# Kernel tuning notes

Measured on AMD Instinct MI355X. Metric: run time of the kernel, lower is better.

## Reference

```python
import jax, jax.numpy as jnp
import numpy as np

E = 16      # num_experts
H = 1024    # hidden_size
O = 1       # output_size
B = 4096    # batch
K = 2       # top-k (hard-coded in module)


def setup_inputs() -> dict:
    key = jax.random.key(0)
    ks = jax.random.split(key, 7)
    s_h = 1.0 / np.sqrt(H)
    inp = {
        "embeddings": jax.random.normal(ks[0], (B, H), dtype=jnp.float32),
        "router_w": jax.random.uniform(ks[1], (H, E), jnp.float32, -s_h, s_h),
        "router_b": jax.random.uniform(ks[2], (E,), jnp.float32, -s_h, s_h),
        "w1": jax.random.uniform(ks[3], (E, H, H), jnp.float32, -s_h, s_h),
        "b1": jax.random.uniform(ks[4], (E, H), jnp.float32, -s_h, s_h),
        "w2": jax.random.uniform(ks[5], (E, H, O), jnp.float32, -s_h, s_h),
        "b2": jax.random.uniform(ks[6], (E, O), jnp.float32, -s_h, s_h),
    }
    return inp


def reference(embeddings, router_w, router_b, w1, b1, w2, b2):
    # Router: top-2 experts per token, softmax over the 2 selected logits.
    logits = embeddings @ router_w + router_b                 # [B, E]
    top_vals, top_idx = jax.lax.top_k(logits, K)              # [B, K]
    top_w = jax.nn.softmax(top_vals, axis=-1)                 # [B, K]

    # Per-expert combine weight: w_e[b] = sum_k top_w[b,k] * (top_idx[b,k]==e)
    onehot = (top_idx[:, :, None] == jnp.arange(E)[None, None, :])  # [B, K, E]
    comb = jnp.einsum('bk,bke->eb', top_w, onehot.astype(top_w.dtype))  # [E, B]

    # Dense per-expert 2-layer MLP (small fixed E); masked-weighted combine
    # reproduces the gather/scatter-add exactly.
    h = jax.nn.relu(jnp.einsum('bh,ehd->ebd', embeddings, w1) + b1[:, None, :])  # [E, B, H]
    out = jnp.einsum('ebd,edo->ebo', h, w2) + b2[:, None, :]                      # [E, B, O]
    prediction = jnp.einsum('eb,ebo->bo', comb, out)                              # [B, O]
    return prediction
```

## Files before the change

### kernel.cpp

```cpp
#include <hip/hip_runtime.h>
#include <hip/hip_bf16.h>
#include <stdint.h>

#define E_EXP 16
#define H_DIM 1024
#define B_TOK 4096
#define NS 4
#define BM 128
#define BN 256
#define BK 64
#define KS 16
#define KC 64
#define RTM 128
#define RSTRIDE (KC + 4)

typedef short bf16x8 __attribute__((ext_vector_type(8)));
typedef float f32x4 __attribute__((ext_vector_type(4)));

__device__ __forceinline__ unsigned short f2bf(float x) {
  union { float f; unsigned u; } v; v.f = x;
  unsigned r = v.u + 0x7FFFu + ((v.u >> 16) & 1u);
  return (unsigned short)(r >> 16);
}

__device__ __forceinline__ void gload_lds16(const void* g, void* l) {
  __builtin_amdgcn_global_load_lds(
      (const __attribute__((address_space(1))) void*)g,
      (__attribute__((address_space(3))) void*)l, 16, 0, 0);
}

__global__ __launch_bounds__(256) void k_router_gemm(
    const float* __restrict__ emb, const float* __restrict__ rw,
    unsigned short* __restrict__ emb_bf, float* __restrict__ part)
{
  __shared__ float embL[RTM * RSTRIDE];
  __shared__ float rwL[KC * E_EXP];

  const int t0 = blockIdx.x * RTM;
  const int ks = blockIdx.y;
  const int tid = threadIdx.x;

#pragma unroll
  for (int it = 0; it < 8; ++it) {
    const int i = tid + 256 * it;
    const int row = i >> 4;
    const int c4 = i & 15;
    const size_t goff = (size_t)(t0 + row) * H_DIM + ks * KC + c4 * 4;
    const f32x4 v = *(const f32x4*)(emb + goff);
    ushort4 o;
    o.x = f2bf(v[0]); o.y = f2bf(v[1]); o.z = f2bf(v[2]); o.w = f2bf(v[3]);
    *(ushort4*)(emb_bf + goff) = o;
    *(f32x4*)(embL + row * RSTRIDE + c4 * 4) = v;
  }
  {
    const f32x4 v = *(const f32x4*)(rw + (size_t)ks * (KC * E_EXP) + tid * 4);
    *(f32x4*)(rwL + tid * 4) = v;
  }
  __syncthreads();

  const int w = tid >> 6, lane = tid & 63;
  const int tg = lane & 15, eg = lane >> 4;
  const int ta = w * 32 + tg, tb = ta + 16;

  f32x4 accA = {0.f, 0.f, 0.f, 0.f};
  f32x4 accB = {0.f, 0.f, 0.f, 0.f};
#pragma unroll
  for (int k4 = 0; k4 < KC / 4; ++k4) {
    const f32x4 e0 = *(const f32x4*)(embL + ta * RSTRIDE + k4 * 4);
    const f32x4 e1 = *(const f32x4*)(embL + tb * RSTRIDE + k4 * 4);
#pragma unroll
    for (int h = 0; h < 4; ++h) {
      const f32x4 r = *(const f32x4*)(rwL + (k4 * 4 + h) * E_EXP + eg * 4);
      accA += e0[h] * r;
      accB += e1[h] * r;
    }
  }

  *(f32x4*)(part + ((size_t)ks * B_TOK + t0 + ta) * E_EXP + eg * 4) = accA;
  *(f32x4*)(part + ((size_t)ks * B_TOK + t0 + tb) * E_EXP + eg * 4) = accB;
}

__global__ __launch_bounds__(256) void k_router_select(
    const float* __restrict__ part, const float* __restrict__ rb,
    int* __restrict__ counts, int* __restrict__ lists,
    int4* __restrict__ meta, float2* __restrict__ wts)
{
  __shared__ int lcnt[E_EXP];
  __shared__ int base[E_EXP];
  const int tid = threadIdx.x;
  const int t = blockIdx.x * 256 + tid;
  if (tid < E_EXP) lcnt[tid] = 0;

  float lg[16];
#pragma unroll
  for (int q = 0; q < 4; ++q) {
    const f32x4 b = *(const f32x4*)(rb + q * 4);
    lg[q * 4 + 0] = b[0]; lg[q * 4 + 1] = b[1];
    lg[q * 4 + 2] = b[2]; lg[q * 4 + 3] = b[3];
  }
#pragma unroll
  for (int s = 0; s < KS; ++s) {
#pragma unroll
    for (int q = 0; q < 4; ++q) {
      const f32x4 v = *(const f32x4*)(part + ((size_t)s * B_TOK + t) * E_EXP + q * 4);
      lg[q * 4 + 0] += v[0]; lg[q * 4 + 1] += v[1];
      lg[q * 4 + 2] += v[2]; lg[q * 4 + 3] += v[3];
    }
  }

  float best = -1e30f; int b0 = 0;
#pragma unroll
  for (int e = 0; e < 16; ++e)
    if (lg[e] > best) { best = lg[e]; b0 = e; }
  float best2 = -1e30f; int b1i = 0;
#pragma unroll
  for (int e = 0; e < 16; ++e)
    if (e != b0 && lg[e] > best2) { best2 = lg[e]; b1i = e; }

  __syncthreads();
  const int l0 = atomicAdd(&lcnt[b0], 1);
  const int l1 = atomicAdd(&lcnt[b1i], 1);
  __syncthreads();
  if (tid < E_EXP) base[tid] = atomicAdd(&counts[tid], lcnt[tid]);
  __syncthreads();

  const int p0 = base[b0] + l0;
  const int p1 = base[b1i] + l1;
  lists[b0 * B_TOK + p0] = t;
  lists[b1i * B_TOK + p1] = t;
  meta[t] = make_int4(b0, b1i, p0, p1);
  const float e1v = expf(best2 - best);
  const float w0 = 1.f / (1.f + e1v);
  wts[t] = make_float2(w0, e1v * w0);
}

__global__ __launch_bounds__(256) void k_w1t(const float* __restrict__ w1,
                                             unsigned short* __restrict__ w1t)
{
  __shared__ unsigned short tile[64][65];
  const int e = blockIdx.z;
  const int ht = blockIdx.x, dt = blockIdx.y;
  const float* src = w1 + ((size_t)e * H_DIM + ht * 64) * H_DIM + dt * 64;
  const int tr = threadIdx.x >> 4;
  const int tc = threadIdx.x & 15;
#pragma unroll
  for (int i = 0; i < 4; ++i) {
    const int r = tr + i * 16;
    const float4 v = *(const float4*)(src + (size_t)r * H_DIM + tc * 4);
    tile[r][tc * 4 + 0] = f2bf(v.x);
    tile[r][tc * 4 + 1] = f2bf(v.y);
    tile[r][tc * 4 + 2] = f2bf(v.z);
    tile[r][tc * 4 + 3] = f2bf(v.w);
  }
  __syncthreads();
  unsigned short* dst = w1t + ((size_t)e * H_DIM + dt * 64) * H_DIM + ht * 64;
  const int wr = threadIdx.x >> 3;
  const int wc = threadIdx.x & 7;
#pragma unroll
  for (int i = 0; i < 2; ++i) {
    const int r = wr + i * 32;
    ushort4 t0, t1;
    t0.x = tile[wc * 8 + 0][r]; t0.y = tile[wc * 8 + 1][r];
    t0.z = tile[wc * 8 + 2][r]; t0.w = tile[wc * 8 + 3][r];
    t1.x = tile[wc * 8 + 4][r]; t1.y = tile[wc * 8 + 5][r];
    t1.z = tile[wc * 8 + 6][r]; t1.w = tile[wc * 8 + 7][r];
    *(ushort4*)(dst + (size_t)r * H_DIM + wc * 8) = t0;
    *(ushort4*)(dst + (size_t)r * H_DIM + wc * 8 + 4) = t1;
  }
}

__global__ __launch_bounds__(512, 4) void k_moe_gemm(
    const unsigned short* __restrict__ emb_bf,
    const unsigned short* __restrict__ w1t,
    const float* __restrict__ b1, const float* __restrict__ w2,
    const int* __restrict__ counts, const int* __restrict__ lists,
    float* __restrict__ outbuf)
{
  const int bid = blockIdx.x;
  const int xcd = bid & 7;
  const int j = bid >> 3;
  const int e = xcd + 8 * (j >> 7);
  const int r = j & 127;
  const int ns = r >> 5;
  const int mb = r & 31;
  const int cnt = counts[e];
  if (mb * BM >= cnt) return;

  __shared__ unsigned short lA[BM * BK];
  __shared__ unsigned short lB[BN * BK];
  __shared__ int toks[BM];

  const int tid = threadIdx.x;
  const int w = tid >> 6, lane = tid & 63;

  if (tid < BM) {
    const int p = mb * BM + tid;
    toks[tid] = lists[e * B_TOK + (p < cnt ? p : 0)];
  }
  __syncthreads();

  const unsigned short* w1te = w1t + ((size_t)e * H_DIM + ns * BN) * H_DIM;

  f32x4 acc[4][4];
#pragma unroll
  for (int m = 0; m < 4; ++m)
#pragma unroll
    for (int n = 0; n < 4; ++n) acc[m][n] = (f32x4){0.f, 0.f, 0.f, 0.f};

  const int scb = ((lane & 7) * 16) ^ ((lane >> 3) << 4);
  const int wm = w >> 2, wn = w & 3;
  const int lr = lane & 15, lg = lane >> 4;

  for (int k0 = 0; k0 < H_DIM; k0 += BK) {
#pragma unroll
    for (int i = 0; i < 2; ++i) {
      const int chunk = w * 2 + i;
      const int row = chunk * 8 + (lane >> 3);
      const unsigned short* src = emb_bf + (size_t)toks[row] * H_DIM + k0 + (scb >> 1);
      gload_lds16(src, (char*)lA + chunk * 1024);
    }
#pragma unroll
    for (int i = 0; i < 4; ++i) {
      const int chunk = w * 4 + i;
      const int n = chunk * 8 + (lane >> 3);
      const unsigned short* src = w1te + (size_t)n * H_DIM + k0 + (scb >> 1);
      gload_lds16(src, (char*)lB + chunk * 1024);
    }
    __syncthreads();

#pragma unroll
    for (int kk = 0; kk < 2; ++kk) {
      const int kb = kk * 64 + lg * 16;
      bf16x8 af[4], bfr[4];
#pragma unroll
      for (int m = 0; m < 4; ++m) {
        const int row = wm * 64 + m * 16 + lr;
        af[m] = *(const bf16x8*)((const char*)lA + row * 128 + (kb ^ ((row & 7) << 4)));
      }
#pragma unroll
      for (int n = 0; n < 4; ++n) {
        const int row = wn * 64 + n * 16 + lr;
        bfr[n] = *(const bf16x8*)((const char*)lB + row * 128 + (kb ^ ((row & 7) << 4)));
      }
#pragma unroll
      for (int m = 0; m < 4; ++m)
#pragma unroll
        for (int n = 0; n < 4; ++n)
          acc[m][n] = __builtin_amdgcn_mfma_f32_16x16x32_bf16(af[m], bfr[n], acc[m][n], 0, 0, 0);
    }
    __syncthreads();
  }

  const float* b1e = b1 + (size_t)e * H_DIM + ns * BN;
  const float* w2e = w2 + (size_t)e * H_DIM + ns * BN;

  float rs[4][4];
#pragma unroll
  for (int m = 0; m < 4; ++m)
#pragma unroll
    for (int r4 = 0; r4 < 4; ++r4) rs[m][r4] = 0.f;

#pragma unroll
  for (int n = 0; n < 4; ++n) {
    const int d = wn * 64 + n * 16 + lr;
    const float bb = b1e[d];
    const float ww = w2e[d];
#pragma unroll
    for (int m = 0; m < 4; ++m)
#pragma unroll
      for (int r4 = 0; r4 < 4; ++r4) {
        float v = acc[m][n][r4] + bb;
        v = fmaxf(v, 0.f);
        rs[m][r4] = fmaf(v, ww, rs[m][r4]);
      }
  }
#pragma unroll
  for (int mask = 8; mask >= 1; mask >>= 1) {
#pragma unroll
    for (int m = 0; m < 4; ++m)
#pragma unroll
      for (int r4 = 0; r4 < 4; ++r4) rs[m][r4] += __shfl_xor(rs[m][r4], mask, 64);
  }

  if (lr == 0) {
    float* ob = outbuf + (((size_t)ns * 4 + wn) * E_EXP + e) * B_TOK + mb * BM;
#pragma unroll
    for (int m = 0; m < 4; ++m)
#pragma unroll
      for (int r4 = 0; r4 < 4; ++r4)
        ob[wm * 64 + m * 16 + lg * 4 + r4] = rs[m][r4];
  }
}

__global__ __launch_bounds__(256) void k_combine(
    const int4* __restrict__ meta, const float2* __restrict__ wts,
    const float* __restrict__ outbuf, const float* __restrict__ b2,
    float* __restrict__ out)
{
  const int t = blockIdx.x * 256 + threadIdx.x;
  if (t >= B_TOK) return;
  const int4 m = meta[t];
  const float2 w = wts[t];
  float o0 = b2[m.x], o1 = b2[m.y];
#pragma unroll
  for (int s = 0; s < NS * 4; ++s) {
    o0 += outbuf[((size_t)s * E_EXP + m.x) * B_TOK + m.z];
    o1 += outbuf[((size_t)s * E_EXP + m.y) * B_TOK + m.w];
  }
  out[t] = w.x * o0 + w.y * o1;
}

extern "C" void kernel_launch(void* const* d_in, const int* in_sizes, int n_in,
                              void* d_out, int out_size, void* d_ws, size_t ws_size,
                              hipStream_t stream)
{
  const float* emb = (const float*)d_in[0];
  const float* rw  = (const float*)d_in[1];
  const float* rb  = (const float*)d_in[2];
  const float* w1  = (const float*)d_in[3];
  const float* b1  = (const float*)d_in[4];
  const float* w2  = (const float*)d_in[5];
  const float* b2  = (const float*)d_in[6];
  float* out = (float*)d_out;

  char* ws = (char*)d_ws;
  size_t cur = 0;
  auto alloc = [&](size_t bytes) -> void* {
    void* p = ws + cur;
    cur += (bytes + 255) & ~(size_t)255;
    return p;
  };
  int*            counts = (int*)alloc(64);
  int4*           meta   = (int4*)alloc((size_t)B_TOK * 16);
  float2*         wts    = (float2*)alloc((size_t)B_TOK * 8);
  int*            lists  = (int*)alloc((size_t)E_EXP * B_TOK * 4);
  float*          outbuf = (float*)alloc((size_t)NS * 4 * E_EXP * B_TOK * 4);
  float*          part   = (float*)alloc((size_t)KS * B_TOK * E_EXP * 4);
  unsigned short* emb_bf = (unsigned short*)alloc((size_t)B_TOK * H_DIM * 2);
  unsigned short* w1t    = (unsigned short*)alloc((size_t)E_EXP * H_DIM * H_DIM * 2);

  hipMemsetAsync(counts, 0, 64, stream);
  k_router_gemm<<<dim3(B_TOK / RTM, KS), 256, 0, stream>>>(emb, rw, emb_bf, part);
  k_router_select<<<B_TOK / 256, 256, 0, stream>>>(part, rb, counts, lists, meta, wts);
  k_w1t<<<dim3(16, 16, 16), 256, 0, stream>>>(w1, w1t);
  k_moe_gemm<<<dim3((B_TOK / BM) * NS * E_EXP), 512, 0, stream>>>(emb_bf, w1t, b1, w2, counts, lists, outbuf);
  k_combine<<<B_TOK / 256, 256, 0, stream>>>(meta, wts, outbuf, b2, out);
}
```

Before: 91.42 us.

## Double-buffer LDS tiles in MoE GEMM to overlap global loads with MFMA

```diff
diff --git a/kernel.cpp b/kernel.cpp
--- a/kernel.cpp
+++ b/kernel.cpp
@@ -169,7 +169,7 @@
   }
 }
 
-__global__ __launch_bounds__(512, 4) void k_moe_gemm(
+__global__ __launch_bounds__(512, 2) void k_moe_gemm(
     const unsigned short* __restrict__ emb_bf,
     const unsigned short* __restrict__ w1t,
     const float* __restrict__ b1, const float* __restrict__ w2,
@@ -186,8 +186,7 @@
   const int cnt = counts[e];
   if (mb * BM >= cnt) return;
 
-  __shared__ unsigned short lA[BM * BK];
-  __shared__ unsigned short lB[BN * BK];
+  __shared__ unsigned short ldsbuf[2][(BM + BN) * BK];
   __shared__ int toks[BM];
 
   const int tid = threadIdx.x;
@@ -201,33 +200,42 @@
 
   const unsigned short* w1te = w1t + ((size_t)e * H_DIM + ns * BN) * H_DIM;
 
+  const int scb = ((lane & 7) * 16) ^ ((lane >> 3) << 4);
+
+  const unsigned short* aSrc[2];
+#pragma unroll
+  for (int i = 0; i < 2; ++i) {
+    const int row = (w * 2 + i) * 8 + (lane >> 3);
+    aSrc[i] = emb_bf + (size_t)toks[row] * H_DIM + (scb >> 1);
+  }
+  const unsigned short* bSrc[4];
+#pragma unroll
+  for (int i = 0; i < 4; ++i) {
+    const int n = (w * 4 + i) * 8 + (lane >> 3);
+    bSrc[i] = w1te + (size_t)n * H_DIM + (scb >> 1);
+  }
+
   f32x4 acc[4][4];
 #pragma unroll
   for (int m = 0; m < 4; ++m)
 #pragma unroll
     for (int n = 0; n < 4; ++n) acc[m][n] = (f32x4){0.f, 0.f, 0.f, 0.f};
 
-  const int scb = ((lane & 7) * 16) ^ ((lane >> 3) << 4);
   const int wm = w >> 2, wn = w & 3;
   const int lr = lane & 15, lg = lane >> 4;
 
-  for (int k0 = 0; k0 < H_DIM; k0 += BK) {
-#pragma unroll
-    for (int i = 0; i < 2; ++i) {
-      const int chunk = w * 2 + i;
-      const int row = chunk * 8 + (lane >> 3);
-      const unsigned short* src = emb_bf + (size_t)toks[row] * H_DIM + k0 + (scb >> 1);
-      gload_lds16(src, (char*)lA + chunk * 1024);
-    }
-#pragma unroll
-    for (int i = 0; i < 4; ++i) {
-      const int chunk = w * 4 + i;
-      const int n = chunk * 8 + (lane >> 3);
-      const unsigned short* src = w1te + (size_t)n * H_DIM + k0 + (scb >> 1);
-      gload_lds16(src, (char*)lB + chunk * 1024);
-    }
-    __syncthreads();
-
+  auto stage = [&](int buf, int k0) {
+    char* base = (char*)ldsbuf[buf];
+#pragma unroll
+    for (int i = 0; i < 2; ++i)
+      gload_lds16(aSrc[i] + k0, base + (w * 2 + i) * 1024);
+#pragma unroll
+    for (int i = 0; i < 4; ++i)
+      gload_lds16(bSrc[i] + k0, base + 16384 + (w * 4 + i) * 1024);
+  };
+
+  auto compute = [&](int buf) {
+    const char* base = (const char*)ldsbuf[buf];
 #pragma unroll
     for (int kk = 0; kk < 2; ++kk) {
       const int kb = kk * 64 + lg * 16;
@@ -235,21 +243,35 @@
 #pragma unroll
       for (int m = 0; m < 4; ++m) {
         const int row = wm * 64 + m * 16 + lr;
-        af[m] = *(const bf16x8*)((const char*)lA + row * 128 + (kb ^ ((row & 7) << 4)));
+        af[m] = *(const bf16x8*)(base + row * 128 + (kb ^ ((row & 7) << 4)));
       }
 #pragma unroll
       for (int n = 0; n < 4; ++n) {
         const int row = wn * 64 + n * 16 + lr;
-        bfr[n] = *(const bf16x8*)((const char*)lB + row * 128 + (kb ^ ((row & 7) << 4)));
+        bfr[n] = *(const bf16x8*)(base + 16384 + row * 128 + (kb ^ ((row & 7) << 4)));
       }
+      __builtin_amdgcn_s_setprio(1);
 #pragma unroll
       for (int m = 0; m < 4; ++m)
 #pragma unroll
         for (int n = 0; n < 4; ++n)
           acc[m][n] = __builtin_amdgcn_mfma_f32_16x16x32_bf16(af[m], bfr[n], acc[m][n], 0, 0, 0);
+      __builtin_amdgcn_s_setprio(0);
     }
+  };
+
+  stage(0, 0);
+  __syncthreads();
+
+  int cur = 0;
+#pragma unroll 1
+  for (int t = 0; t < H_DIM / BK - 1; ++t) {
+    stage(cur ^ 1, (t + 1) * BK);
+    compute(cur);
     __syncthreads();
-  }
+    cur ^= 1;
+  }
+  compute(cur);
 
   const float* b1e = b1 + (size_t)e * H_DIM + ns * BN;
   const float* w2e = w2 + (size_t)e * H_DIM + ns * BN;
```

Result: no change. 90.43 us (-1.1%).

## Restructure MoE GEMM into persistent 128x64 tiles looping over token blocks

Applied to the files above, without the earlier changes.

```diff
diff --git a/kernel.cpp b/kernel.cpp
--- a/kernel.cpp
+++ b/kernel.cpp
@@ -5,10 +5,10 @@
 #define E_EXP 16
 #define H_DIM 1024
 #define B_TOK 4096
-#define NS 4
-#define BM 128
-#define BN 256
 #define BK 64
+#define GBM 128
+#define GBN 64
+#define NSLOT 32
 #define KS 16
 #define KC 64
 #define RTM 128
@@ -169,7 +169,7 @@
   }
 }
 
-__global__ __launch_bounds__(512, 4) void k_moe_gemm(
+__global__ __launch_bounds__(256, 4) void k_moe_gemm(
     const unsigned short* __restrict__ emb_bf,
     const unsigned short* __restrict__ w1t,
     const float* __restrict__ b1, const float* __restrict__ w2,
@@ -179,116 +179,125 @@
   const int bid = blockIdx.x;
   const int xcd = bid & 7;
   const int j = bid >> 3;
-  const int e = xcd + 8 * (j >> 7);
-  const int r = j & 127;
-  const int ns = r >> 5;
-  const int mb = r & 31;
+  const int e  = xcd + 8 * (j >> 7);
+  const int r  = j & 127;
+  const int nb = r >> 3;
+  const int mbg = r & 7;
   const int cnt = counts[e];
-  if (mb * BM >= cnt) return;
-
-  __shared__ unsigned short lA[BM * BK];
-  __shared__ unsigned short lB[BN * BK];
-  __shared__ int toks[BM];
+
+  __shared__ unsigned short lA[GBM * BK];
+  __shared__ unsigned short lB[GBN * BK];
+  __shared__ int toks[GBM];
 
   const int tid = threadIdx.x;
   const int w = tid >> 6, lane = tid & 63;
-
-  if (tid < BM) {
-    const int p = mb * BM + tid;
-    toks[tid] = lists[e * B_TOK + (p < cnt ? p : 0)];
-  }
-  __syncthreads();
-
-  const unsigned short* w1te = w1t + ((size_t)e * H_DIM + ns * BN) * H_DIM;
-
-  f32x4 acc[4][4];
-#pragma unroll
-  for (int m = 0; m < 4; ++m)
-#pragma unroll
-    for (int n = 0; n < 4; ++n) acc[m][n] = (f32x4){0.f, 0.f, 0.f, 0.f};
-
   const int scb = ((lane & 7) * 16) ^ ((lane >> 3) << 4);
-  const int wm = w >> 2, wn = w & 3;
+  const int wm = w >> 1, wn = w & 1;
   const int lr = lane & 15, lg = lane >> 4;
 
-  for (int k0 = 0; k0 < H_DIM; k0 += BK) {
-#pragma unroll
-    for (int i = 0; i < 2; ++i) {
-      const int chunk = w * 2 + i;
-      const int row = chunk * 8 + (lane >> 3);
-      const unsigned short* src = emb_bf + (size_t)toks[row] * H_DIM + k0 + (scb >> 1);
-      gload_lds16(src, (char*)lA + chunk * 1024);
-    }
+  const unsigned short* w1tb = w1t + ((size_t)e * H_DIM + nb * GBN) * H_DIM;
+  const float* b1e = b1 + (size_t)e * H_DIM + nb * GBN;
+  const float* w2e = w2 + (size_t)e * H_DIM + nb * GBN;
+
+  const unsigned short* bSrc[2];
+#pragma unroll
+  for (int i = 0; i < 2; ++i) {
+    const int n = (w * 2 + i) * 8 + (lane >> 3);
+    bSrc[i] = w1tb + (size_t)n * H_DIM + (scb >> 1);
+  }
+
+  for (int mb = mbg; mb * GBM < cnt; mb += 8) {
+    if (tid < GBM) {
+      const int p = mb * GBM + tid;
+      toks[tid] = lists[e * B_TOK + (p < cnt ? p : 0)];
+    }
+    __syncthreads();
+
+    const unsigned short* aSrc[4];
 #pragma unroll
     for (int i = 0; i < 4; ++i) {
-      const int chunk = w * 4 + i;
-      const int n = chunk * 8 + (lane >> 3);
-      const unsigned short* src = w1te + (size_t)n * H_DIM + k0 + (scb >> 1);
-      gload_lds16(src, (char*)lB + chunk * 1024);
+      const int row = (w * 4 + i) * 8 + (lane >> 3);
+      aSrc[i] = emb_bf + (size_t)toks[row] * H_DIM + (scb >> 1);
+    }
+
+    f32x4 acc[4][2];
+#pragma unroll
+    for (int m = 0; m < 4; ++m)
+#pragma unroll
+      for (int n = 0; n < 2; ++n) acc[m][n] = (f32x4){0.f, 0.f, 0.f, 0.f};
+
+    for (int k0 = 0; k0 < H_DIM; k0 += BK) {
+#pragma unroll
+      for (int i = 0; i < 4; ++i)
+        gload_lds16(aSrc[i] + k0, (char*)lA + (w * 4 + i) * 1024);
+#pragma unroll
+      for (int i = 0; i < 2; ++i)
+        gload_lds16(bSrc[i] + k0, (char*)lB + (w * 2 + i) * 1024);
+      __syncthreads();
+
+#pragma unroll
+      for (int kk = 0; kk < 2; ++kk) {
+        const int kb = kk * 64 + lg * 16;
+        bf16x8 af[4], bfr[2];
+#pragma unroll
+        for (int m = 0; m < 4; ++m) {
+          const int row = wm * 64 + m * 16 + lr;
+          af[m] = *(const bf16x8*)((const char*)lA + row * 128 + (kb ^ ((row & 7) << 4)));
+        }
+#pragma unroll
+        for (int n = 0; n < 2; ++n) {
+          const int row = wn * 32 + n * 16 + lr;
+          bfr[n] = *(const bf16x8*)((const char*)lB + row * 128 + (kb ^ ((row & 7) << 4)));
+        }
+        __builtin_amdgcn_s_setprio(1);
+#pragma unroll
+        for (int m = 0; m < 4; ++m)
+#pragma unroll
+          for (int n = 0; n < 2; ++n)
+            acc[m][n] = __builtin_amdgcn_mfma_f32_16x16x32_bf16(af[m], bfr[n], acc[m][n], 0, 0, 0);
+        __builtin_amdgcn_s_setprio(0);
+      }
+      __syncthreads();
+    }
+
+    float rs[4][4];
+#pragma unroll
+    for (int m = 0; m < 4; ++m)
+#pragma unroll
+      for (int r4 = 0; r4 < 4; ++r4) rs[m][r4] = 0.f;
+
+#pragma unroll
+    for (int n = 0; n < 2; ++n) {
+      const int d = wn * 32 + n * 16 + lr;
+      const float bb = b1e[d];
+      const float ww = w2e[d];
+#pragma unroll
+      for (int m = 0; m < 4; ++m)
+#pragma unroll
+        for (int r4 = 0; r4 < 4; ++r4) {
+          float v = acc[m][n][r4] + bb;
+          v = fmaxf(v, 0.f);
+          rs[m][r4] = fmaf(v, ww, rs[m][r4]);
+        }
+    }
+#pragma unroll
+    for (int mask = 8; mask >= 1; mask >>= 1) {
+#pragma unroll
+      for (int m = 0; m < 4; ++m)
+#pragma unroll
+        for (int r4 = 0; r4 < 4; ++r4) rs[m][r4] += __shfl_xor(rs[m][r4], mask, 64);
+    }
+
+    if (lr == 0) {
+      const int slot = nb * 2 + wn;
+      float* ob = outbuf + ((size_t)slot * E_EXP + e) * B_TOK + mb * GBM;
+#pragma unroll
+      for (int m = 0; m < 4; ++m)
+#pragma unroll
+        for (int r4 = 0; r4 < 4; ++r4)
+          ob[wm * 64 + m * 16 + lg * 4 + r4] = rs[m][r4];
     }
     __syncthreads();
-
-#pragma unroll
-    for (int kk = 0; kk < 2; ++kk) {
-      const int kb = kk * 64 + lg * 16;
-      bf16x8 af[4], bfr[4];
-#pragma unroll
-      for (int m = 0; m < 4; ++m) {
-        const int row = wm * 64 + m * 16 + lr;
-        af[m] = *(const bf16x8*)((const char*)lA + row * 128 + (kb ^ ((row & 7) << 4)));
-      }
-#pragma unroll
-      for (int n = 0; n < 4; ++n) {
-        const int row = wn * 64 + n * 16 + lr;
-        bfr[n] = *(const bf16x8*)((const char*)lB + row * 128 + (kb ^ ((row & 7) << 4)));
-      }
-#pragma unroll
-      for (int m = 0; m < 4; ++m)
-#pragma unroll
-        for (int n = 0; n < 4; ++n)
-          acc[m][n] = __builtin_amdgcn_mfma_f32_16x16x32_bf16(af[m], bfr[n], acc[m][n], 0, 0, 0);
-    }
-    __syncthreads();
-  }
-
-  const float* b1e = b1 + (size_t)e * H_DIM + ns * BN;
-  const float* w2e = w2 + (size_t)e * H_DIM + ns * BN;
-
-  float rs[4][4];
-#pragma unroll
-  for (int m = 0; m < 4; ++m)
-#pragma unroll
-    for (int r4 = 0; r4 < 4; ++r4) rs[m][r4] = 0.f;
-
-#pragma unroll
-  for (int n = 0; n < 4; ++n) {
-    const int d = wn * 64 + n * 16 + lr;
-    const float bb = b1e[d];
-    const float ww = w2e[d];
-#pragma unroll
-    for (int m = 0; m < 4; ++m)
-#pragma unroll
-      for (int r4 = 0; r4 < 4; ++r4) {
-        float v = acc[m][n][r4] + bb;
-        v = fmaxf(v, 0.f);
-        rs[m][r4] = fmaf(v, ww, rs[m][r4]);
-      }
-  }
-#pragma unroll
-  for (int mask = 8; mask >= 1; mask >>= 1) {
-#pragma unroll
-    for (int m = 0; m < 4; ++m)
-#pragma unroll
-      for (int r4 = 0; r4 < 4; ++r4) rs[m][r4] += __shfl_xor(rs[m][r4], mask, 64);
-  }
-
-  if (lr == 0) {
-    float* ob = outbuf + (((size_t)ns * 4 + wn) * E_EXP + e) * B_TOK + mb * BM;
-#pragma unroll
-    for (int m = 0; m < 4; ++m)
-#pragma unroll
-      for (int r4 = 0; r4 < 4; ++r4)
-        ob[wm * 64 + m * 16 + lg * 4 + r4] = rs[m][r4];
   }
 }
 
@@ -303,7 +312,7 @@
   const float2 w = wts[t];
   float o0 = b2[m.x], o1 = b2[m.y];
 #pragma unroll
-  for (int s = 0; s < NS * 4; ++s) {
+  for (int s = 0; s < NSLOT; ++s) {
     o0 += outbuf[((size_t)s * E_EXP + m.x) * B_TOK + m.z];
     o1 += outbuf[((size_t)s * E_EXP + m.y) * B_TOK + m.w];
   }
@@ -334,7 +343,7 @@
   int4*           meta   = (int4*)alloc((size_t)B_TOK * 16);
   float2*         wts    = (float2*)alloc((size_t)B_TOK * 8);
   int*            lists  = (int*)alloc((size_t)E_EXP * B_TOK * 4);
-  float*          outbuf = (float*)alloc((size_t)NS * 4 * E_EXP * B_TOK * 4);
+  float*          outbuf = (float*)alloc((size_t)NSLOT * E_EXP * B_TOK * 4);
   float*          part   = (float*)alloc((size_t)KS * B_TOK * E_EXP * 4);
   unsigned short* emb_bf = (unsigned short*)alloc((size_t)B_TOK * H_DIM * 2);
   unsigned short* w1t    = (unsigned short*)alloc((size_t)E_EXP * H_DIM * H_DIM * 2);
@@ -343,6 +352,6 @@
   k_router_gemm<<<dim3(B_TOK / RTM, KS), 256, 0, stream>>>(emb, rw, emb_bf, part);
   k_router_select<<<B_TOK / 256, 256, 0, stream>>>(part, rb, counts, lists, meta, wts);
   k_w1t<<<dim3(16, 16, 16), 256, 0, stream>>>(w1, w1t);
-  k_moe_gemm<<<dim3((B_TOK / BM) * NS * E_EXP), 512, 0, stream>>>(emb_bf, w1t, b1, w2, counts, lists, outbuf);
+  k_moe_gemm<<<dim3(2048), 256, 0, stream>>>(emb_bf, w1t, b1, w2, counts, lists, outbuf);
   k_combine<<<B_TOK / 256, 256, 0, stream>>>(meta, wts, outbuf, b2, out);
 }
```

New measurement: 88.32 us. 3.4% less time.

## Keep W1 column slab resident in LDS and stream tokens from global

Applied to the files above, without the earlier changes.

```diff
diff --git a/kernel.cpp b/kernel.cpp
--- a/kernel.cpp
+++ b/kernel.cpp
@@ -5,10 +5,8 @@
 #define E_EXP 16
 #define H_DIM 1024
 #define B_TOK 4096
-#define NS 4
-#define BM 128
-#define BN 256
-#define BK 64
+#define GBN 64
+#define NSLOT 16
 #define KS 16
 #define KC 64
 #define RTM 128
@@ -169,7 +167,7 @@
   }
 }
 
-__global__ __launch_bounds__(512, 4) void k_moe_gemm(
+__global__ __launch_bounds__(512, 2) void k_moe_gemm(
     const unsigned short* __restrict__ emb_bf,
     const unsigned short* __restrict__ w1t,
     const float* __restrict__ b1, const float* __restrict__ w2,
@@ -177,118 +175,102 @@
     float* __restrict__ outbuf)
 {
   const int bid = blockIdx.x;
-  const int xcd = bid & 7;
-  const int j = bid >> 3;
-  const int e = xcd + 8 * (j >> 7);
-  const int r = j & 127;
-  const int ns = r >> 5;
-  const int mb = r & 31;
+  const int e  = (bid & 7) + 8 * ((bid >> 3) & 1);
+  const int nb = bid >> 4;
   const int cnt = counts[e];
-  if (mb * BM >= cnt) return;
-
-  __shared__ unsigned short lA[BM * BK];
-  __shared__ unsigned short lB[BN * BK];
-  __shared__ int toks[BM];
+
+  __shared__ unsigned short lB[GBN * H_DIM];
 
   const int tid = threadIdx.x;
   const int w = tid >> 6, lane = tid & 63;
-
-  if (tid < BM) {
-    const int p = mb * BM + tid;
-    toks[tid] = lists[e * B_TOK + (p < cnt ? p : 0)];
-  }
-  __syncthreads();
-
-  const unsigned short* w1te = w1t + ((size_t)e * H_DIM + ns * BN) * H_DIM;
-
-  f32x4 acc[4][4];
-#pragma unroll
-  for (int m = 0; m < 4; ++m)
-#pragma unroll
-    for (int n = 0; n < 4; ++n) acc[m][n] = (f32x4){0.f, 0.f, 0.f, 0.f};
-
-  const int scb = ((lane & 7) * 16) ^ ((lane >> 3) << 4);
-  const int wm = w >> 2, wn = w & 3;
   const int lr = lane & 15, lg = lane >> 4;
 
-  for (int k0 = 0; k0 < H_DIM; k0 += BK) {
-#pragma unroll
-    for (int i = 0; i < 2; ++i) {
-      const int chunk = w * 2 + i;
-      const int row = chunk * 8 + (lane >> 3);
-      const unsigned short* src = emb_bf + (size_t)toks[row] * H_DIM + k0 + (scb >> 1);
-      gload_lds16(src, (char*)lA + chunk * 1024);
-    }
-#pragma unroll
-    for (int i = 0; i < 4; ++i) {
-      const int chunk = w * 4 + i;
-      const int n = chunk * 8 + (lane >> 3);
-      const unsigned short* src = w1te + (size_t)n * H_DIM + k0 + (scb >> 1);
-      gload_lds16(src, (char*)lB + chunk * 1024);
-    }
-    __syncthreads();
-
-#pragma unroll
-    for (int kk = 0; kk < 2; ++kk) {
-      const int kb = kk * 64 + lg * 16;
+  const unsigned short* w1tb = w1t + ((size_t)e * H_DIM + nb * GBN) * H_DIM;
+
+#pragma unroll
+  for (int i = 0; i < 16; ++i) {
+    const int c = w * 16 + i;
+    const int n = c >> 1, half = c & 1;
+    const int sb = (half * 1024 + lane * 16) ^ ((n & 7) << 4);
+    gload_lds16((const char*)w1tb + n * 2048 + sb, (char*)lB + c * 1024);
+  }
+  __syncthreads();
+
+  const float* b1e = b1 + (size_t)e * H_DIM + nb * GBN;
+  const float* w2e = w2 + (size_t)e * H_DIM + nb * GBN;
+
+  for (int base = w * 64; base < cnt; base += 512) {
+    const unsigned short* aP[4];
+#pragma unroll
+    for (int m = 0; m < 4; ++m) {
+      const int p = base + m * 16 + lr;
+      const int tok = lists[e * B_TOK + (p < cnt ? p : 0)];
+      aP[m] = emb_bf + (size_t)tok * H_DIM + lg * 8;
+    }
+
+    f32x4 acc[4][4];
+#pragma unroll
+    for (int m = 0; m < 4; ++m)
+#pragma unroll
+      for (int n = 0; n < 4; ++n) acc[m][n] = (f32x4){0.f, 0.f, 0.f, 0.f};
+
+#pragma unroll 8
+    for (int kk = 0; kk < 32; ++kk) {
       bf16x8 af[4], bfr[4];
 #pragma unroll
-      for (int m = 0; m < 4; ++m) {
-        const int row = wm * 64 + m * 16 + lr;
-        af[m] = *(const bf16x8*)((const char*)lA + row * 128 + (kb ^ ((row & 7) << 4)));
+      for (int m = 0; m < 4; ++m)
+        af[m] = *(const bf16x8*)(aP[m] + kk * 32);
+#pragma unroll
+      for (int j = 0; j < 4; ++j) {
+        const int col = j * 16 + lr;
+        bfr[j] = *(const bf16x8*)((const char*)lB + col * 2048 +
+                                  ((kk * 64 + lg * 16) ^ ((col & 7) << 4)));
       }
-#pragma unroll
-      for (int n = 0; n < 4; ++n) {
-        const int row = wn * 64 + n * 16 + lr;
-        bfr[n] = *(const bf16x8*)((const char*)lB + row * 128 + (kb ^ ((row & 7) << 4)));
-      }
+      __builtin_amdgcn_s_setprio(1);
 #pragma unroll
       for (int m = 0; m < 4; ++m)
 #pragma unroll
         for (int n = 0; n < 4; ++n)
           acc[m][n] = __builtin_amdgcn_mfma_f32_16x16x32_bf16(af[m], bfr[n], acc[m][n], 0, 0, 0);
-    }
-    __syncthreads();
-  }
-
-  const float* b1e = b1 + (size_t)e * H_DIM + ns * BN;
-  const float* w2e = w2 + (size_t)e * H_DIM + ns * BN;
-
-  float rs[4][4];
-#pragma unroll
-  for (int m = 0; m < 4; ++m)
-#pragma unroll
-    for (int r4 = 0; r4 < 4; ++r4) rs[m][r4] = 0.f;
-
-#pragma unroll
-  for (int n = 0; n < 4; ++n) {
-    const int d = wn * 64 + n * 16 + lr;
-    const float bb = b1e[d];
-    const float ww = w2e[d];
+      __builtin_amdgcn_s_setprio(0);
+    }
+
+    float rs[4][4];
 #pragma unroll
     for (int m = 0; m < 4; ++m)
 #pragma unroll
-      for (int r4 = 0; r4 < 4; ++r4) {
-        float v = acc[m][n][r4] + bb;
-        v = fmaxf(v, 0.f);
-        rs[m][r4] = fmaf(v, ww, rs[m][r4]);
-      }
-  }
-#pragma unroll
-  for (int mask = 8; mask >= 1; mask >>= 1) {
-#pragma unroll
-    for (int m = 0; m < 4; ++m)
-#pragma unroll
-      for (int r4 = 0; r4 < 4; ++r4) rs[m][r4] += __shfl_xor(rs[m][r4], mask, 64);
-  }
-
-  if (lr == 0) {
-    float* ob = outbuf + (((size_t)ns * 4 + wn) * E_EXP + e) * B_TOK + mb * BM;
-#pragma unroll
-    for (int m = 0; m < 4; ++m)
-#pragma unroll
-      for (int r4 = 0; r4 < 4; ++r4)
-        ob[wm * 64 + m * 16 + lg * 4 + r4] = rs[m][r4];
+      for (int r4 = 0; r4 < 4; ++r4) rs[m][r4] = 0.f;
+
+#pragma unroll
+    for (int j = 0; j < 4; ++j) {
+      const int d = j * 16 + lr;
+      const float bb = b1e[d];
+      const float ww = w2e[d];
+#pragma unroll
+      for (int m = 0; m < 4; ++m)
+#pragma unroll
+        for (int r4 = 0; r4 < 4; ++r4) {
+          float v = acc[m][j][r4] + bb;
+          v = fmaxf(v, 0.f);
+          rs[m][r4] = fmaf(v, ww, rs[m][r4]);
+        }
+    }
+#pragma unroll
+    for (int mask = 8; mask >= 1; mask >>= 1) {
+#pragma unroll
+      for (int m = 0; m < 4; ++m)
+#pragma unroll
+        for (int r4 = 0; r4 < 4; ++r4) rs[m][r4] += __shfl_xor(rs[m][r4], mask, 64);
+    }
+
+    if (lr == 0) {
+      float* ob = outbuf + ((size_t)nb * E_EXP + e) * B_TOK + base;
+#pragma unroll
+      for (int m = 0; m < 4; ++m)
+#pragma unroll
+        for (int r4 = 0; r4 < 4; ++r4)
+          ob[m * 16 + lg * 4 + r4] = rs[m][r4];
+    }
   }
 }
 
@@ -303,7 +285,7 @@
   const float2 w = wts[t];
   float o0 = b2[m.x], o1 = b2[m.y];
 #pragma unroll
-  for (int s = 0; s < NS * 4; ++s) {
+  for (int s = 0; s < NSLOT; ++s) {
     o0 += outbuf[((size_t)s * E_EXP + m.x) * B_TOK + m.z];
     o1 += outbuf[((size_t)s * E_EXP + m.y) * B_TOK + m.w];
   }
@@ -334,7 +316,7 @@
   int4*           meta   = (int4*)alloc((size_t)B_TOK * 16);
   float2*         wts    = (float2*)alloc((size_t)B_TOK * 8);
   int*            lists  = (int*)alloc((size_t)E_EXP * B_TOK * 4);
-  float*          outbuf = (float*)alloc((size_t)NS * 4 * E_EXP * B_TOK * 4);
+  float*          outbuf = (float*)alloc((size_t)NSLOT * E_EXP * B_TOK * 4);
   float*          part   = (float*)alloc((size_t)KS * B_TOK * E_EXP * 4);
   unsigned short* emb_bf = (unsigned short*)alloc((size_t)B_TOK * H_DIM * 2);
   unsigned short* w1t    = (unsigned short*)alloc((size_t)E_EXP * H_DIM * H_DIM * 2);
@@ -343,6 +325,6 @@
   k_router_gemm<<<dim3(B_TOK / RTM, KS), 256, 0, stream>>>(emb, rw, emb_bf, part);
   k_router_select<<<B_TOK / 256, 256, 0, stream>>>(part, rb, counts, lists, meta, wts);
   k_w1t<<<dim3(16, 16, 16), 256, 0, stream>>>(w1, w1t);
-  k_moe_gemm<<<dim3((B_TOK / BM) * NS * E_EXP), 512, 0, stream>>>(emb_bf, w1t, b1, w2, counts, lists, outbuf);
+  k_moe_gemm<<<dim3(256), 512, 0, stream>>>(emb_bf, w1t, b1, w2, counts, lists, outbuf);
   k_combine<<<B_TOK / 256, 256, 0, stream>>>(meta, wts, outbuf, b2, out);
 }
```

New measurement: 93.93 us. 2.8% more time.
